# Optimization experiments

Hardware: AMD Instinct MI355X
Metric: run time of the kernel (lower is better)

The kernel has to match this reference:

```python
import jax, jax.numpy as jnp
import numpy as np

B = 4096
M = 4            # n_modalities
T = 8            # n_tasks
D = 1024         # feature_dim per modality
DIN = D * M      # concat feature dim = 4096
H = 256          # hidden_dim
H2 = 2 * H       # 512
TEMP = 1.0
EPS = 1e-5


def _layernorm(x, g, b):
    # LayerNorm over last axis (torch nn.LayerNorm semantics, eps=1e-5)
    mu = jnp.mean(x, axis=-1, keepdims=True)
    var = jnp.mean(jnp.square(x - mu), axis=-1, keepdims=True)
    return (x - mu) * jax.lax.rsqrt(var + EPS) * g + b


def setup_inputs() -> dict:
    key = jax.random.key(0)
    ks = jax.random.split(key, 16)
    s = 0.02
    return {
        "f0": jax.random.normal(ks[0], (B, D), jnp.float32),
        "f1": jax.random.normal(ks[1], (B, D), jnp.float32),
        "f2": jax.random.normal(ks[2], (B, D), jnp.float32),
        "f3": jax.random.normal(ks[3], (B, D), jnp.float32),
        # per-task feature-net params (stacked ModuleList)
        "W1": jax.random.normal(ks[4], (T, DIN, H2), jnp.float32) * s,
        "b1": jnp.zeros((T, H2), jnp.float32),
        "g1": jnp.ones((T, H2), jnp.float32),
        "be1": jnp.zeros((T, H2), jnp.float32),
        "W2": jax.random.normal(ks[5], (T, H2, H), jnp.float32) * s,
        "b2": jnp.zeros((T, H), jnp.float32),
        "g2": jnp.ones((T, H), jnp.float32),
        "be2": jnp.zeros((T, H), jnp.float32),
        "task_emb": jax.random.normal(ks[6], (T, H), jnp.float32),
        # per-task weight-net params (Linear(2H -> M))
        "Ww": jax.random.normal(ks[7], (T, H2, M), jnp.float32) * s,
        "bw": jnp.zeros((T, M), jnp.float32),
        "task_ids": jax.random.randint(ks[8], (B,), 0, T, jnp.int32),
    }


def reference(f0, f1, f2, f3, W1, b1, g1, be1, W2, b2, g2, be2, task_emb, Ww, bw, task_ids):
    x = jnp.concatenate([f0, f1, f2, f3], axis=1)              # [B, DIN]
    # compute all-task feature nets densely (T is small), then gather per sample
    h = jnp.einsum('bd,tdh->bth', x, W1) + b1[None]            # [B, T, 2H]
    h = jax.nn.relu(_layernorm(h, g1[None], be1[None]))
    h = jnp.einsum('bth,thk->btk', h, W2) + b2[None]           # [B, T, H]
    h = jax.nn.relu(_layernorm(h, g2[None], be2[None]))
    hid = jnp.take_along_axis(h, task_ids[:, None, None], axis=1)[:, 0]  # [B, H]
    te = task_emb[task_ids]                                    # [B, H]
    comb = jnp.concatenate([hid, te], axis=1)                  # [B, 2H]
    # per-sample gather of small weight-net matrices (irregular access)
    raw = jnp.einsum('bh,bhm->bm', comb, Ww[task_ids]) + bw[task_ids]    # [B, M]
    return jax.nn.softmax(raw / TEMP, axis=1)
```

## Files before the change

kernel.cpp:

```cpp
#include <hip/hip_runtime.h>
#include <stdint.h>

#define B_N 4096
#define T_N 8
#define DIN 4096
#define H2C 512
#define HC 256
#define NWG1 1024
#define NWG2 264
#define SPLITK1 4

typedef __attribute__((ext_vector_type(8))) short bf16x8;
typedef __attribute__((ext_vector_type(4))) float f32x4;

static __device__ __forceinline__ unsigned short f2bf(float f) {
    union { float f; uint32_t u; } v; v.f = f;
    uint32_t u = v.u;
    uint32_t r = (u + 0x7FFFu + ((u >> 16) & 1u)) >> 16;
    return (unsigned short)r;
}

static __device__ __forceinline__ float bf2f(uint32_t h) {
    union { uint32_t u; float f; } v; v.u = h << 16; return v.f;
}

static __device__ __forceinline__ uint32_t pk2(float a, float b) {
    uint32_t r;
    asm volatile("v_cvt_pk_bf16_f32 %0, %1, %2" : "=v"(r) : "v"(a), "v"(b));
    return r;
}

static __device__ __forceinline__ void gl2lds16(const unsigned short* g, unsigned short* l) {
    __builtin_amdgcn_global_load_lds(
        (const __attribute__((address_space(1))) unsigned int*)(g),
        (__attribute__((address_space(3))) unsigned int*)(l), 16, 0, 0);
}

static __device__ __forceinline__ int xcd_remap(int bid, int nwg) {
    int xcd = bid & 7, idx = bid >> 3;
    int q = nwg >> 3, r = nwg & 7;
    return (xcd < r ? xcd * (q + 1) : r * (q + 1) + (xcd - r) * q) + idx;
}

__launch_bounds__(256)
__global__ void k_pre(const float* __restrict__ f0, const float* __restrict__ f1,
                      const float* __restrict__ f2, const float* __restrict__ f3,
                      const float* __restrict__ W1, const float* __restrict__ W2,
                      const int* __restrict__ task_ids,
                      const float* __restrict__ temb, const float* __restrict__ Ww,
                      const float* __restrict__ bw,
                      unsigned short* __restrict__ Xb, unsigned short* __restrict__ W1t,
                      unsigned short* __restrict__ W2t,
                      int* __restrict__ order, int* __restrict__ tiles, int* __restrict__ bmap,
                      int* __restrict__ tiles2, int* __restrict__ ntile2,
                      float* __restrict__ tb) {
    int blk = blockIdx.x, tid = threadIdx.x;
    if (blk == 0) {
        __shared__ unsigned long long wtot[4][2];
        __shared__ int lc[T_N], lseg[T_N], tb1p[T_N + 1], tb2p[T_N + 1];
        int lane = tid & 63, wv = tid >> 6;
        int4 a0 = *(const int4*)(task_ids + tid * 16);
        int4 a1 = *(const int4*)(task_ids + tid * 16 + 4);
        int4 a2 = *(const int4*)(task_ids + tid * 16 + 8);
        int4 a3 = *(const int4*)(task_ids + tid * 16 + 12);
        int myt[16] = {a0.x, a0.y, a0.z, a0.w, a1.x, a1.y, a1.z, a1.w,
                       a2.x, a2.y, a2.z, a2.w, a3.x, a3.y, a3.z, a3.w};
        unsigned long long ph0 = 0, ph1 = 0;
        #pragma unroll
        for (int i = 0; i < 16; ++i) {
            int t = myt[i];
            if (t < 4) ph0 += 1ull << (t * 16); else ph1 += 1ull << ((t - 4) * 16);
        }
        unsigned long long s0 = ph0, s1 = ph1;
        for (int o = 1; o < 64; o <<= 1) {
            unsigned long long u0 = __shfl_up(s0, o);
            unsigned long long u1 = __shfl_up(s1, o);
            if (lane >= o) { s0 += u0; s1 += u1; }
        }
        if (lane == 63) { wtot[wv][0] = s0; wtot[wv][1] = s1; }
        __syncthreads();
        unsigned long long e0 = s0 - ph0, e1 = s1 - ph1;
        for (int w2 = 0; w2 < wv; ++w2) { e0 += wtot[w2][0]; e1 += wtot[w2][1]; }
        if (tid == 0) {
            unsigned long long t0 = 0, t1 = 0;
            for (int w2 = 0; w2 < 4; ++w2) { t0 += wtot[w2][0]; t1 += wtot[w2][1]; }
            int s = 0;
            for (int t = 0; t < T_N; ++t) {
                int c = (int)((t < 4 ? (t0 >> (t * 16)) : (t1 >> ((t - 4) * 16))) & 0xFFFF);
                lc[t] = c; lseg[t] = s; s += c;
            }
            int q1 = 0, q2 = 0;
            for (int t = 0; t < T_N; ++t) {
                tb1p[t] = q1; tb2p[t] = q2;
                q1 += (lc[t] + 127) >> 7; q2 += (lc[t] + 15) >> 4;
            }
            tb1p[T_N] = q1; tb2p[T_N] = q2;
            ntile2[0] = q2;
        }
        __syncthreads();
        unsigned long long r0 = e0, r1 = e1;
        #pragma unroll
        for (int i = 0; i < 16; ++i) {
            int t = myt[i], rk;
            if (t < 4) { rk = (int)((r0 >> (t * 16)) & 0xFFFF); r0 += 1ull << (t * 16); }
            else { int u = t - 4; rk = (int)((r1 >> (u * 16)) & 0xFFFF); r1 += 1ull << (u * 16); }
            order[lseg[t] + rk] = tid * 16 + i;
        }
        int n1 = tb1p[T_N], n2 = tb2p[T_N];
        for (int e = tid; e < n1; e += 256) {
            int t = 0; while (e >= tb1p[t + 1]) ++t;
            int rr = (e - tb1p[t]) << 7;
            tiles[3 * e] = t; tiles[3 * e + 1] = lseg[t] + rr;
            int rem = lc[t] - rr; tiles[3 * e + 2] = rem < 128 ? rem : 128;
        }
        for (int e = tid; e < n2; e += 256) {
            int t = 0; while (e >= tb2p[t + 1]) ++t;
            int rr = (e - tb2p[t]) << 4;
            tiles2[3 * e] = t; tiles2[3 * e + 1] = lseg[t] + rr;
            int rem = lc[t] - rr; tiles2[3 * e + 2] = rem < 16 ? rem : 16;
        }
        for (int s = tid; s < NWG1; s += 256) {
            int t = s & 7, j = s >> 3;
            int base = tb1p[t], nt = tb1p[t + 1] - base;
            bmap[s] = (j < nt * 16) ? (((base + (j >> 4)) << 4) | (j & 15)) : -1;
        }
        __syncthreads();
        if (tid == 0) {
            int freeslot = 0;
            for (int t = 0; t < T_N; ++t) {
                int base = tb1p[t], nt = tb1p[t + 1] - base;
                for (int j = 128; j < nt * 16; ++j) {
                    while (bmap[freeslot] >= 0) ++freeslot;
                    bmap[freeslot] = ((base + (j >> 4)) << 4) | (j & 15);
                }
            }
        }
        for (int t = wv; t < T_N; t += 4) {
            int m = lane & 3, hb = (lane >> 2) * 16;
            float s = 0.f;
            for (int h = 0; h < 16; ++h)
                s += temb[t * HC + hb + h] * Ww[((size_t)t * H2C + HC + hb + h) * 4 + m];
            for (int o = 4; o < 64; o <<= 1) s += __shfl_xor(s, o);
            if (lane < 4) tb[t * 4 + lane] = s + bw[t * 4 + lane];
        }
        return;
    }
    if (blk <= 8192) {
        int g = (blk - 1) * 256 + tid;
        int b = g >> 9, col = (g & 511) * 8;
        int m = col >> 10, d = col & 1023;
        const float* s = (m == 0) ? f0 : (m == 1) ? f1 : (m == 2) ? f2 : f3;
        const float4* sp = (const float4*)(s + (size_t)b * 1024 + d);
        float4 a = sp[0], c = sp[1];
        uint4 w;
        w.x = pk2(a.x, a.y); w.y = pk2(a.z, a.w);
        w.z = pk2(c.x, c.y); w.w = pk2(c.z, c.w);
        *(uint4*)(Xb + (size_t)b * DIN + col) = w;
        return;
    }
    __shared__ float tile[64][65];
    const float* ip; unsigned short* op; int R, C, bx, by, t;
    if (blk < 12289) {
        int idx = blk - 8193; bx = idx & 63; by = (idx >> 6) & 7; t = idx >> 9;
        R = DIN; C = H2C;
        ip = W1 + (size_t)t * R * C; op = W1t + (size_t)t * R * C;
    } else {
        int idx = blk - 12289; bx = idx & 7; by = (idx >> 3) & 3; t = idx >> 5;
        R = H2C; C = HC;
        ip = W2 + (size_t)t * R * C; op = W2t + (size_t)t * R * C;
    }
    int r0 = bx * 64, c0 = by * 64;
    int lr = tid >> 4, lc4 = (tid & 15) * 4;
    #pragma unroll
    for (int i = 0; i < 4; ++i) {
        float4 v = *(const float4*)&ip[(size_t)(r0 + lr + i * 16) * C + c0 + lc4];
        tile[lr + i * 16][lc4 + 0] = v.x;
        tile[lr + i * 16][lc4 + 1] = v.y;
        tile[lr + i * 16][lc4 + 2] = v.z;
        tile[lr + i * 16][lc4 + 3] = v.w;
    }
    __syncthreads();
    int r4 = (tid & 15) * 4;
    #pragma unroll
    for (int i = 0; i < 4; ++i) {
        int cc = i * 16 + (tid >> 4);
        uint2 wv;
        wv.x = pk2(tile[r4 + 0][cc], tile[r4 + 1][cc]);
        wv.y = pk2(tile[r4 + 2][cc], tile[r4 + 3][cc]);
        *(uint2*)&op[(size_t)(c0 + cc) * R + r0 + r4] = wv;
    }
}

__launch_bounds__(256)
__global__ void k_gemm1(const unsigned short* __restrict__ A, const unsigned short* __restrict__ Bt,
                        unsigned short* __restrict__ Cb16, const int* __restrict__ order,
                        const int* __restrict__ tiles, const int* __restrict__ bmap) {
    int e = bmap[blockIdx.x];
    if (e < 0) return;
    int tix = e >> 4, sub = e & 15;
    int ct = sub >> 2, kc = sub & 3;
    int t = tiles[3 * tix], prow = tiles[3 * tix + 1], rows = tiles[3 * tix + 2];
    int kb = kc * (DIN / SPLITK1);

    __shared__ unsigned short lds[2][16384];

    int tid = threadIdx.x, lane = tid & 63, w = tid >> 6;
    int wm = w >> 1, wn = w & 1;

    const unsigned short* pA[4];
    const unsigned short* pB[4];
    #pragma unroll
    for (int j = 0; j < 4; ++j) {
        int row = j * 32 + (tid >> 3);
        int colg = (tid & 7) ^ (row & 7);
        int rl = row < rows ? row : rows - 1;
        pA[j] = A + (size_t)order[prow + rl] * DIN + kb + colg * 8;
        pB[j] = Bt + ((size_t)t * H2C + ct * 128 + row) * DIN + kb + colg * 8;
    }

    f32x4 acc[4][4];
    #pragma unroll
    for (int m = 0; m < 4; ++m)
        #pragma unroll
        for (int n = 0; n < 4; ++n)
            acc[m][n] = (f32x4){0.f, 0.f, 0.f, 0.f};

    auto stage = [&](int buf, int k0) {
        unsigned short* dA = &lds[buf][w * 512];
        unsigned short* dB = dA + 8192;
        #pragma unroll
        for (int j = 0; j < 4; ++j) gl2lds16(pA[j] + k0, dA + j * 2048);
        #pragma unroll
        for (int j = 0; j < 4; ++j) gl2lds16(pB[j] + k0, dB + j * 2048);
    };

    constexpr int NIT = DIN / SPLITK1 / 64;
    stage(0, 0);
    __syncthreads();
    int cur = 0;
    for (int it = 0; it < NIT; ++it) {
        if (it + 1 < NIT) stage(cur ^ 1, (it + 1) * 64);
        const unsigned short* As = &lds[cur][0];
        const unsigned short* Bs = As + 8192;
        #pragma unroll
        for (int ks = 0; ks < 2; ++ks) {
            int g = ks * 4 + (lane >> 4);
            bf16x8 af[4], bfv[4];
            #pragma unroll
            for (int m = 0; m < 4; ++m) {
                int row = wm * 64 + m * 16 + (lane & 15);
                af[m] = *(const bf16x8*)&As[row * 64 + ((g ^ (row & 7)) * 8)];
            }
            #pragma unroll
            for (int n = 0; n < 4; ++n) {
                int row = wn * 64 + n * 16 + (lane & 15);
                bfv[n] = *(const bf16x8*)&Bs[row * 64 + ((g ^ (row & 7)) * 8)];
            }
            #pragma unroll
            for (int m = 0; m < 4; ++m)
                #pragma unroll
                for (int n = 0; n < 4; ++n)
                    acc[m][n] = __builtin_amdgcn_mfma_f32_16x16x32_bf16(af[m], bfv[n], acc[m][n], 0, 0, 0);
        }
        __syncthreads();
        cur ^= 1;
    }

    unsigned short* Cb = Cb16 + (size_t)kc * B_N * H2C;
    #pragma unroll
    for (int m = 0; m < 4; ++m) {
        #pragma unroll
        for (int n = 0; n < 4; ++n) {
            int col = ct * 128 + wn * 64 + n * 16 + (lane & 15);
            #pragma unroll
            for (int j = 0; j < 4; ++j) {
                int row = wm * 64 + m * 16 + (lane >> 4) * 4 + j;
                if (row < rows)
                    Cb[(size_t)(prow + row) * H2C + col] = f2bf(acc[m][n][j]);
            }
        }
    }
}

__launch_bounds__(256)
__global__ void k_gemm2f(const unsigned short* __restrict__ h1p, const unsigned short* __restrict__ W2t,
                         const float* __restrict__ b1, const float* __restrict__ g1,
                         const float* __restrict__ be1,
                         const float* __restrict__ b2, const float* __restrict__ g2,
                         const float* __restrict__ be2,
                         const float* __restrict__ Ww, const float* __restrict__ tb,
                         const int* __restrict__ order,
                         const int* __restrict__ tiles2, const int* __restrict__ ntile2,
                         float* __restrict__ out) {
    __shared__ unsigned short Asm[16 * 512];
    __shared__ unsigned short Bsm[2][256 * 32];
    __shared__ float red[16][4][4];

    int id = xcd_remap(blockIdx.x, NWG2);
    if (id >= ntile2[0]) return;
    int t = tiles2[3 * id], prow = tiles2[3 * id + 1], rows = tiles2[3 * id + 2];
    int tid = threadIdx.x, lane = tid & 63, w = tid >> 6;

    {
        int r = tid >> 4;
        int rl = r < rows ? r : rows - 1;
        int c0 = (tid & 15) * 32;
        const unsigned short* p0 = h1p + (size_t)(prow + rl) * H2C + c0;
        const float* pb = b1 + t * H2C + c0;
        float x[32];
        float s = 0.f, sq = 0.f;
        #pragma unroll
        for (int i = 0; i < 32; i += 8) {
            uint4 u0 = *(const uint4*)(p0 + i);
            uint4 u1 = *(const uint4*)(p0 + (size_t)B_N * H2C + i);
            uint4 u2 = *(const uint4*)(p0 + (size_t)2 * B_N * H2C + i);
            uint4 u3 = *(const uint4*)(p0 + (size_t)3 * B_N * H2C + i);
            uint32_t w0[4] = {u0.x, u0.y, u0.z, u0.w};
            uint32_t w1[4] = {u1.x, u1.y, u1.z, u1.w};
            uint32_t w2[4] = {u2.x, u2.y, u2.z, u2.w};
            uint32_t w3[4] = {u3.x, u3.y, u3.z, u3.w};
            float4 c0v = *(const float4*)(pb + i);
            float4 c1v = *(const float4*)(pb + i + 4);
            float cv[8] = {c0v.x, c0v.y, c0v.z, c0v.w, c1v.x, c1v.y, c1v.z, c1v.w};
            #pragma unroll
            for (int q = 0; q < 4; ++q) {
                float v0 = bf2f(w0[q] & 0xFFFFu) + bf2f(w1[q] & 0xFFFFu)
                         + bf2f(w2[q] & 0xFFFFu) + bf2f(w3[q] & 0xFFFFu) + cv[2 * q];
                float v1 = bf2f(w0[q] >> 16) + bf2f(w1[q] >> 16)
                         + bf2f(w2[q] >> 16) + bf2f(w3[q] >> 16) + cv[2 * q + 1];
                x[i + 2 * q] = v0; x[i + 2 * q + 1] = v1;
                s += v0 + v1; sq += v0 * v0 + v1 * v1;
            }
        }
        #pragma unroll
        for (int o = 1; o < 16; o <<= 1) { s += __shfl_xor(s, o); sq += __shfl_xor(sq, o); }
        float mean = s * (1.f / H2C);
        float var = sq * (1.f / H2C) - mean * mean;
        float rstd = rsqrtf(var + 1e-5f);
        const float* pg = g1 + t * H2C + c0;
        const float* pe = be1 + t * H2C + c0;
        #pragma unroll
        for (int i = 0; i < 32; i += 8) {
            float yv[8];
            #pragma unroll
            for (int q = 0; q < 8; q += 4) {
                float4 gv = *(const float4*)(pg + i + q);
                float4 ev = *(const float4*)(pe + i + q);
                yv[q + 0] = fmaxf((x[i + q + 0] - mean) * rstd * gv.x + ev.x, 0.f);
                yv[q + 1] = fmaxf((x[i + q + 1] - mean) * rstd * gv.y + ev.y, 0.f);
                yv[q + 2] = fmaxf((x[i + q + 2] - mean) * rstd * gv.z + ev.z, 0.f);
                yv[q + 3] = fmaxf((x[i + q + 3] - mean) * rstd * gv.w + ev.w, 0.f);
            }
            uint4 wv;
            wv.x = pk2(yv[0], yv[1]); wv.y = pk2(yv[2], yv[3]);
            wv.z = pk2(yv[4], yv[5]); wv.w = pk2(yv[6], yv[7]);
            int g = (c0 + i) >> 3;
            *(uint4*)&Asm[r * 512 + ((g ^ (r & 7)) * 8)] = wv;
        }
    }

    auto stageB = [&](int buf, int it) {
        #pragma unroll
        for (int j = 0; j < 4; ++j) {
            int G = j * 256 + tid;
            int row = G >> 2, g = G & 3;
            int colg = g ^ (row & 3);
            gl2lds16(W2t + ((size_t)t * HC + row) * H2C + it * 32 + colg * 8,
                     &Bsm[buf][(j * 256 + w * 64) * 8]);
        }
    };

    stageB(0, 0);
    __syncthreads();

    f32x4 acc[4];
    #pragma unroll
    for (int n = 0; n < 4; ++n) acc[n] = (f32x4){0.f, 0.f, 0.f, 0.f};

    for (int it = 0; it < 16; ++it) {
        if (it + 1 < 16) stageB((it + 1) & 1, it + 1);
        const unsigned short* Bs = &Bsm[it & 1][0];
        int g = lane >> 4;
        int arow = lane & 15;
        bf16x8 af = *(const bf16x8*)&Asm[arow * 512 + (((it * 4 + g) ^ (arow & 7)) * 8)];
        #pragma unroll
        for (int n = 0; n < 4; ++n) {
            int brow = w * 64 + n * 16 + arow;
            bf16x8 bv = *(const bf16x8*)&Bs[brow * 32 + ((g ^ (brow & 3)) * 8)];
            acc[n] = __builtin_amdgcn_mfma_f32_16x16x32_bf16(af, bv, acc[n], 0, 0, 0);
        }
        __syncthreads();
    }

    float b2v[4], g2v[4], e2v[4];
    float4 wv[4];
    #pragma unroll
    for (int n = 0; n < 4; ++n) {
        int col = w * 64 + n * 16 + (lane & 15);
        b2v[n] = b2[t * HC + col];
        g2v[n] = g2[t * HC + col];
        e2v[n] = be2[t * HC + col];
        wv[n] = *(const float4*)&Ww[((size_t)t * H2C + col) * 4];
    }
    float s4[4], q4[4];
    #pragma unroll
    for (int j = 0; j < 4; ++j) {
        float s = 0.f, sq = 0.f;
        #pragma unroll
        for (int n = 0; n < 4; ++n) {
            float xv = acc[n][j] + b2v[n];
            s += xv; sq += xv * xv;
        }
        #pragma unroll
        for (int o = 1; o < 16; o <<= 1) { s += __shfl_xor(s, o); sq += __shfl_xor(sq, o); }
        s4[j] = s; q4[j] = sq;
    }
    if ((lane & 15) == 0) {
        #pragma unroll
        for (int j = 0; j < 4; ++j) {
            int r = (lane >> 4) * 4 + j;
            red[r][w][0] = s4[j];
            red[r][w][1] = q4[j];
        }
    }
    __syncthreads();
    float mean[4], rstd[4];
    #pragma unroll
    for (int j = 0; j < 4; ++j) {
        int r = (lane >> 4) * 4 + j;
        float S = red[r][0][0] + red[r][1][0] + red[r][2][0] + red[r][3][0];
        float SQ = red[r][0][1] + red[r][1][1] + red[r][2][1] + red[r][3][1];
        mean[j] = S * (1.f / HC);
        float var = SQ * (1.f / HC) - mean[j] * mean[j];
        rstd[j] = rsqrtf(var + 1e-5f);
    }
    float p[4][4];
    #pragma unroll
    for (int j = 0; j < 4; ++j) {
        p[j][0] = 0.f; p[j][1] = 0.f; p[j][2] = 0.f; p[j][3] = 0.f;
        #pragma unroll
        for (int n = 0; n < 4; ++n) {
            float yv = fmaxf((acc[n][j] + b2v[n] - mean[j]) * rstd[j] * g2v[n] + e2v[n], 0.f);
            p[j][0] += yv * wv[n].x; p[j][1] += yv * wv[n].y;
            p[j][2] += yv * wv[n].z; p[j][3] += yv * wv[n].w;
        }
        #pragma unroll
        for (int m = 0; m < 4; ++m)
            #pragma unroll
            for (int o = 1; o < 16; o <<= 1) p[j][m] += __shfl_xor(p[j][m], o);
    }
    __syncthreads();
    if ((lane & 15) == 0) {
        #pragma unroll
        for (int j = 0; j < 4; ++j) {
            int r = (lane >> 4) * 4 + j;
            red[r][w][0] = p[j][0]; red[r][w][1] = p[j][1];
            red[r][w][2] = p[j][2]; red[r][w][3] = p[j][3];
        }
    }
    __syncthreads();
    if (tid < 16 && tid < rows) {
        float raw[4];
        #pragma unroll
        for (int m = 0; m < 4; ++m)
            raw[m] = red[tid][0][m] + red[tid][1][m] + red[tid][2][m] + red[tid][3][m] + tb[t * 4 + m];
        float mx = fmaxf(fmaxf(raw[0], raw[1]), fmaxf(raw[2], raw[3]));
        float e0 = expf(raw[0] - mx), e1 = expf(raw[1] - mx);
        float e2 = expf(raw[2] - mx), e3 = expf(raw[3] - mx);
        float si = 1.f / (e0 + e1 + e2 + e3);
        *(float4*)(out + (size_t)order[prow + tid] * 4) = make_float4(e0 * si, e1 * si, e2 * si, e3 * si);
    }
}

extern "C" void kernel_launch(void* const* d_in, const int* in_sizes, int n_in,
                              void* d_out, int out_size, void* d_ws, size_t ws_size,
                              hipStream_t stream) {
    const float* f0 = (const float*)d_in[0];
    const float* f1 = (const float*)d_in[1];
    const float* f2 = (const float*)d_in[2];
    const float* f3 = (const float*)d_in[3];
    const float* W1 = (const float*)d_in[4];
    const float* b1 = (const float*)d_in[5];
    const float* g1 = (const float*)d_in[6];
    const float* be1 = (const float*)d_in[7];
    const float* W2 = (const float*)d_in[8];
    const float* b2 = (const float*)d_in[9];
    const float* g2 = (const float*)d_in[10];
    const float* be2 = (const float*)d_in[11];
    const float* temb = (const float*)d_in[12];
    const float* Ww = (const float*)d_in[13];
    const float* bw = (const float*)d_in[14];
    const int* task_ids = (const int*)d_in[15];
    float* out = (float*)d_out;

    char* ws = (char*)d_ws;
    size_t off = 0;
    auto walloc = [&](size_t bytes) -> void* {
        void* p = ws + off;
        off = (off + bytes + 255) & ~(size_t)255;
        return p;
    };
    float* tb = (float*)walloc(128);
    int* tiles = (int*)walloc(64 * 3 * 4);
    int* bmap = (int*)walloc(NWG1 * 4);
    int* tiles2 = (int*)walloc(272 * 3 * 4);
    int* ntile2 = (int*)walloc(4);
    int* order = (int*)walloc((size_t)B_N * 4);
    unsigned short* Xb = (unsigned short*)walloc((size_t)B_N * DIN * 2);
    unsigned short* W1t = (unsigned short*)walloc((size_t)T_N * H2C * DIN * 2);
    unsigned short* W2t = (unsigned short*)walloc((size_t)T_N * HC * H2C * 2);
    unsigned short* h1p = (unsigned short*)walloc((size_t)SPLITK1 * B_N * H2C * 2);

    k_pre<<<12545, 256, 0, stream>>>(f0, f1, f2, f3, W1, W2, task_ids, temb, Ww, bw,
                                     Xb, W1t, W2t, order, tiles, bmap, tiles2, ntile2, tb);
    k_gemm1<<<NWG1, 256, 0, stream>>>(Xb, W1t, h1p, order, tiles, bmap);
    k_gemm2f<<<NWG2, 256, 0, stream>>>(h1p, W2t, b1, g1, be1, b2, g2, be2, Ww, tb,
                                       order, tiles2, ntile2, out);
}
```

Baseline: 91.39 us.

## Coarsen prep kernel blocks, drop LDS staging of W2 in GEMM2, grid by task

```diff
diff --git a/kernel.cpp b/kernel.cpp
--- a/kernel.cpp
+++ b/kernel.cpp
@@ -7,7 +7,7 @@
 #define H2C 512
 #define HC 256
 #define NWG1 1024
-#define NWG2 264
+#define NWG2 2048
 #define SPLITK1 4
 
 typedef __attribute__((ext_vector_type(8))) short bf16x8;
@@ -24,22 +24,10 @@
     union { uint32_t u; float f; } v; v.u = h << 16; return v.f;
 }
 
-static __device__ __forceinline__ uint32_t pk2(float a, float b) {
-    uint32_t r;
-    asm volatile("v_cvt_pk_bf16_f32 %0, %1, %2" : "=v"(r) : "v"(a), "v"(b));
-    return r;
-}
-
 static __device__ __forceinline__ void gl2lds16(const unsigned short* g, unsigned short* l) {
     __builtin_amdgcn_global_load_lds(
         (const __attribute__((address_space(1))) unsigned int*)(g),
         (__attribute__((address_space(3))) unsigned int*)(l), 16, 0, 0);
-}
-
-static __device__ __forceinline__ int xcd_remap(int bid, int nwg) {
-    int xcd = bid & 7, idx = bid >> 3;
-    int q = nwg >> 3, r = nwg & 7;
-    return (xcd < r ? xcd * (q + 1) : r * (q + 1) + (xcd - r) * q) + idx;
 }
 
 __launch_bounds__(256)
@@ -52,7 +40,7 @@
                       unsigned short* __restrict__ Xb, unsigned short* __restrict__ W1t,
                       unsigned short* __restrict__ W2t,
                       int* __restrict__ order, int* __restrict__ tiles, int* __restrict__ bmap,
-                      int* __restrict__ tiles2, int* __restrict__ ntile2,
+                      int* __restrict__ tiles2, int* __restrict__ tbp,
                       float* __restrict__ tb) {
     int blk = blockIdx.x, tid = threadIdx.x;
     if (blk == 0) {
@@ -95,7 +83,6 @@
                 q1 += (lc[t] + 127) >> 7; q2 += (lc[t] + 15) >> 4;
             }
             tb1p[T_N] = q1; tb2p[T_N] = q2;
-            ntile2[0] = q2;
         }
         __syncthreads();
         unsigned long long r0 = e0, r1 = e1;
@@ -106,6 +93,7 @@
             else { int u = t - 4; rk = (int)((r1 >> (u * 16)) & 0xFFFF); r1 += 1ull << (u * 16); }
             order[lseg[t] + rk] = tid * 16 + i;
         }
+        if (tid <= T_N) tbp[tid] = tb2p[tid];
         int n1 = tb1p[T_N], n2 = tb2p[T_N];
         for (int e = tid; e < n1; e += 256) {
             int t = 0; while (e >= tb1p[t + 1]) ++t;
@@ -145,49 +133,66 @@
         }
         return;
     }
-    if (blk <= 8192) {
-        int g = (blk - 1) * 256 + tid;
-        int b = g >> 9, col = (g & 511) * 8;
+    if (blk <= 2048) {
+        int g0 = ((blk - 1) * 256 + tid) * 4;
+        size_t e0 = (size_t)g0 * 8;
+        int b = (int)(e0 >> 12), col = (int)(e0 & 4095);
         int m = col >> 10, d = col & 1023;
         const float* s = (m == 0) ? f0 : (m == 1) ? f1 : (m == 2) ? f2 : f3;
         const float4* sp = (const float4*)(s + (size_t)b * 1024 + d);
-        float4 a = sp[0], c = sp[1];
-        uint4 w;
-        w.x = pk2(a.x, a.y); w.y = pk2(a.z, a.w);
-        w.z = pk2(c.x, c.y); w.w = pk2(c.z, c.w);
-        *(uint4*)(Xb + (size_t)b * DIN + col) = w;
+        unsigned short* op = Xb + (size_t)b * DIN + col;
+        #pragma unroll
+        for (int q = 0; q < 4; ++q) {
+            float4 a = sp[2 * q], c = sp[2 * q + 1];
+            uint4 w;
+            w.x = (uint32_t)f2bf(a.x) | ((uint32_t)f2bf(a.y) << 16);
+            w.y = (uint32_t)f2bf(a.z) | ((uint32_t)f2bf(a.w) << 16);
+            w.z = (uint32_t)f2bf(c.x) | ((uint32_t)f2bf(c.y) << 16);
+            w.w = (uint32_t)f2bf(c.z) | ((uint32_t)f2bf(c.w) << 16);
+            *(uint4*)(op + q * 8) = w;
+        }
         return;
     }
-    __shared__ float tile[64][65];
-    const float* ip; unsigned short* op; int R, C, bx, by, t;
-    if (blk < 12289) {
-        int idx = blk - 8193; bx = idx & 63; by = (idx >> 6) & 7; t = idx >> 9;
+    __shared__ float tile[128 * 65];
+    const float* ip; unsigned short* op; int R, C, r0, c0;
+    if (blk <= 4096) {
+        int idx = blk - 2049;
+        int bx = idx & 31, by = (idx >> 5) & 7, t = idx >> 8;
         R = DIN; C = H2C;
         ip = W1 + (size_t)t * R * C; op = W1t + (size_t)t * R * C;
+        r0 = bx * 128; c0 = by * 64;
     } else {
-        int idx = blk - 12289; bx = idx & 7; by = (idx >> 3) & 3; t = idx >> 5;
+        int idx = blk - 4097;
+        int bx = idx & 3, by = (idx >> 2) & 3, t = idx >> 4;
         R = H2C; C = HC;
         ip = W2 + (size_t)t * R * C; op = W2t + (size_t)t * R * C;
-    }
-    int r0 = bx * 64, c0 = by * 64;
-    int lr = tid >> 4, lc4 = (tid & 15) * 4;
-    #pragma unroll
-    for (int i = 0; i < 4; ++i) {
-        float4 v = *(const float4*)&ip[(size_t)(r0 + lr + i * 16) * C + c0 + lc4];
-        tile[lr + i * 16][lc4 + 0] = v.x;
-        tile[lr + i * 16][lc4 + 1] = v.y;
-        tile[lr + i * 16][lc4 + 2] = v.z;
-        tile[lr + i * 16][lc4 + 3] = v.w;
+        r0 = bx * 128; c0 = by * 64;
+    }
+    {
+        int kq = tid >> 4, c4 = (tid & 15) * 4;
+        #pragma unroll
+        for (int i = 0; i < 8; ++i) {
+            int k = kq + i * 16;
+            float4 v = *(const float4*)&ip[(size_t)(r0 + k) * C + c0 + c4];
+            int q = (k >> 5) & 3;
+            tile[k * 65 + ((c4 + 0) ^ q)] = v.x;
+            tile[k * 65 + ((c4 + 1) ^ q)] = v.y;
+            tile[k * 65 + ((c4 + 2) ^ q)] = v.z;
+            tile[k * 65 + ((c4 + 3) ^ q)] = v.w;
+        }
     }
     __syncthreads();
-    int r4 = (tid & 15) * 4;
-    #pragma unroll
-    for (int i = 0; i < 4; ++i) {
-        int cc = i * 16 + (tid >> 4);
-        uint2 wv;
-        wv.x = pk2(tile[r4 + 0][cc], tile[r4 + 1][cc]);
-        wv.y = pk2(tile[r4 + 2][cc], tile[r4 + 3][cc]);
-        *(uint2*)&op[(size_t)(c0 + cc) * R + r0 + r4] = wv;
+    {
+        int col = tid >> 2, q = tid & 3;
+        int colS = col ^ q;
+        unsigned short ow[32];
+        #pragma unroll
+        for (int j = 0; j < 32; ++j)
+            ow[j] = f2bf(tile[(q * 32 + j) * 65 + colS]);
+        unsigned short* dst = op + (size_t)(c0 + col) * R + r0 + q * 32;
+        #pragma unroll
+        for (int v = 0; v < 4; ++v)
+            *(uint4*)(dst + v * 8) = *(uint4*)&ow[v * 8];
     }
 }
 
@@ -290,15 +295,16 @@
                          const float* __restrict__ be2,
                          const float* __restrict__ Ww, const float* __restrict__ tb,
                          const int* __restrict__ order,
-                         const int* __restrict__ tiles2, const int* __restrict__ ntile2,
+                         const int* __restrict__ tiles2, const int* __restrict__ tbp,
                          float* __restrict__ out) {
     __shared__ unsigned short Asm[16 * 512];
-    __shared__ unsigned short Bsm[2][256 * 32];
     __shared__ float red[16][4][4];
 
-    int id = xcd_remap(blockIdx.x, NWG2);
-    if (id >= ntile2[0]) return;
-    int t = tiles2[3 * id], prow = tiles2[3 * id + 1], rows = tiles2[3 * id + 2];
+    int tres = blockIdx.x & 7, j = blockIdx.x >> 3;
+    int base = tbp[tres];
+    if (base + j >= tbp[tres + 1]) return;
+    int e = base + j;
+    int t = tiles2[3 * e], prow = tiles2[3 * e + 1], rows = tiles2[3 * e + 2];
     int tid = threadIdx.x, lane = tid & 63, w = tid >> 6;
 
     {
@@ -341,55 +347,46 @@
         const float* pe = be1 + t * H2C + c0;
         #pragma unroll
         for (int i = 0; i < 32; i += 8) {
-            float yv[8];
+            unsigned short y[8];
             #pragma unroll
             for (int q = 0; q < 8; q += 4) {
                 float4 gv = *(const float4*)(pg + i + q);
                 float4 ev = *(const float4*)(pe + i + q);
-                yv[q + 0] = fmaxf((x[i + q + 0] - mean) * rstd * gv.x + ev.x, 0.f);
-                yv[q + 1] = fmaxf((x[i + q + 1] - mean) * rstd * gv.y + ev.y, 0.f);
-                yv[q + 2] = fmaxf((x[i + q + 2] - mean) * rstd * gv.z + ev.z, 0.f);
-                yv[q + 3] = fmaxf((x[i + q + 3] - mean) * rstd * gv.w + ev.w, 0.f);
+                y[q + 0] = f2bf(fmaxf((x[i + q + 0] - mean) * rstd * gv.x + ev.x, 0.f));
+                y[q + 1] = f2bf(fmaxf((x[i + q + 1] - mean) * rstd * gv.y + ev.y, 0.f));
+                y[q + 2] = f2bf(fmaxf((x[i + q + 2] - mean) * rstd * gv.z + ev.z, 0.f));
+                y[q + 3] = f2bf(fmaxf((x[i + q + 3] - mean) * rstd * gv.w + ev.w, 0.f));
             }
             uint4 wv;
-            wv.x = pk2(yv[0], yv[1]); wv.y = pk2(yv[2], yv[3]);
-            wv.z = pk2(yv[4], yv[5]); wv.w = pk2(yv[6], yv[7]);
+            wv.x = (uint32_t)y[0] | ((uint32_t)y[1] << 16);
+            wv.y = (uint32_t)y[2] | ((uint32_t)y[3] << 16);
+            wv.z = (uint32_t)y[4] | ((uint32_t)y[5] << 16);
+            wv.w = (uint32_t)y[6] | ((uint32_t)y[7] << 16);
             int g = (c0 + i) >> 3;
             *(uint4*)&Asm[r * 512 + ((g ^ (r & 7)) * 8)] = wv;
         }
     }
-
-    auto stageB = [&](int buf, int it) {
-        #pragma unroll
-        for (int j = 0; j < 4; ++j) {
-            int G = j * 256 + tid;
-            int row = G >> 2, g = G & 3;
-            int colg = g ^ (row & 3);
-            gl2lds16(W2t + ((size_t)t * HC + row) * H2C + it * 32 + colg * 8,
-                     &Bsm[buf][(j * 256 + w * 64) * 8]);
-        }
-    };
-
-    stageB(0, 0);
     __syncthreads();
 
+    int g = lane >> 4, arow = lane & 15;
+    const unsigned short* bp[4];
+    #pragma unroll
+    for (int n = 0; n < 4; ++n)
+        bp[n] = W2t + ((size_t)t * HC + w * 64 + n * 16 + arow) * H2C + g * 8;
+
     f32x4 acc[4];
     #pragma unroll
     for (int n = 0; n < 4; ++n) acc[n] = (f32x4){0.f, 0.f, 0.f, 0.f};
 
+    #pragma unroll 4
     for (int it = 0; it < 16; ++it) {
-        if (it + 1 < 16) stageB((it + 1) & 1, it + 1);
-        const unsigned short* Bs = &Bsm[it & 1][0];
-        int g = lane >> 4;
-        int arow = lane & 15;
         bf16x8 af = *(const bf16x8*)&Asm[arow * 512 + (((it * 4 + g) ^ (arow & 7)) * 8)];
-        #pragma unroll
-        for (int n = 0; n < 4; ++n) {
-            int brow = w * 64 + n * 16 + arow;
-            bf16x8 bv = *(const bf16x8*)&Bs[brow * 32 + ((g ^ (brow & 3)) * 8)];
-            acc[n] = __builtin_amdgcn_mfma_f32_16x16x32_bf16(af, bv, acc[n], 0, 0, 0);
-        }
-        __syncthreads();
+        bf16x8 bv[4];
+        #pragma unroll
+        for (int n = 0; n < 4; ++n) bv[n] = *(const bf16x8*)(bp[n] + it * 32);
+        #pragma unroll
+        for (int n = 0; n < 4; ++n)
+            acc[n] = __builtin_amdgcn_mfma_f32_16x16x32_bf16(af, bv[n], acc[n], 0, 0, 0);
     }
 
     float b2v[4], g2v[4], e2v[4];
@@ -404,58 +401,58 @@
     }
     float s4[4], q4[4];
     #pragma unroll
-    for (int j = 0; j < 4; ++j) {
+    for (int j2 = 0; j2 < 4; ++j2) {
         float s = 0.f, sq = 0.f;
         #pragma unroll
         for (int n = 0; n < 4; ++n) {
-            float xv = acc[n][j] + b2v[n];
+            float xv = acc[n][j2] + b2v[n];
             s += xv; sq += xv * xv;
         }
         #pragma unroll
         for (int o = 1; o < 16; o <<= 1) { s += __shfl_xor(s, o); sq += __shfl_xor(sq, o); }
-        s4[j] = s; q4[j] = sq;
+        s4[j2] = s; q4[j2] = sq;
     }
     if ((lane & 15) == 0) {
         #pragma unroll
-        for (int j = 0; j < 4; ++j) {
-            int r = (lane >> 4) * 4 + j;
-            red[r][w][0] = s4[j];
-            red[r][w][1] = q4[j];
+        for (int j2 = 0; j2 < 4; ++j2) {
+            int r = (lane >> 4) * 4 + j2;
+            red[r][w][0] = s4[j2];
+            red[r][w][1] = q4[j2];
         }
     }
     __syncthreads();
     float mean[4], rstd[4];
     #pragma unroll
-    for (int j = 0; j < 4; ++j) {
-        int r = (lane >> 4) * 4 + j;
+    for (int j2 = 0; j2 < 4; ++j2) {
+        int r = (lane >> 4) * 4 + j2;
         float S = red[r][0][0] + red[r][1][0] + red[r][2][0] + red[r][3][0];
         float SQ = red[r][0][1] + red[r][1][1] + red[r][2][1] + red[r][3][1];
-        mean[j] = S * (1.f / HC);
-        float var = SQ * (1.f / HC) - mean[j] * mean[j];
-        rstd[j] = rsqrtf(var + 1e-5f);
+        mean[j2] = S * (1.f / HC);
+        float var = SQ * (1.f / HC) - mean[j2] * mean[j2];
+        rstd[j2] = rsqrtf(var + 1e-5f);
     }
     float p[4][4];
     #pragma unroll
-    for (int j = 0; j < 4; ++j) {
-        p[j][0] = 0.f; p[j][1] = 0.f; p[j][2] = 0.f; p[j][3] = 0.f;
+    for (int j2 = 0; j2 < 4; ++j2) {
+        p[j2][0] = 0.f; p[j2][1] = 0.f; p[j2][2] = 0.f; p[j2][3] = 0.f;
         #pragma unroll
         for (int n = 0; n < 4; ++n) {
-            float yv = fmaxf((acc[n][j] + b2v[n] - mean[j]) * rstd[j] * g2v[n] + e2v[n], 0.f);
-            p[j][0] += yv * wv[n].x; p[j][1] += yv * wv[n].y;
-            p[j][2] += yv * wv[n].z; p[j][3] += yv * wv[n].w;
+            float yv = fmaxf((acc[n][j2] + b2v[n] - mean[j2]) * rstd[j2] * g2v[n] + e2v[n], 0.f);
+            p[j2][0] += yv * wv[n].x; p[j2][1] += yv * wv[n].y;
+            p[j2][2] += yv * wv[n].z; p[j2][3] += yv * wv[n].w;
         }
         #pragma unroll
         for (int m = 0; m < 4; ++m)
             #pragma unroll
-            for (int o = 1; o < 16; o <<= 1) p[j][m] += __shfl_xor(p[j][m], o);
+            for (int o = 1; o < 16; o <<= 1) p[j2][m] += __shfl_xor(p[j2][m], o);
     }
     __syncthreads();
     if ((lane & 15) == 0) {
         #pragma unroll
-        for (int j = 0; j < 4; ++j) {
-            int r = (lane >> 4) * 4 + j;
-            red[r][w][0] = p[j][0]; red[r][w][1] = p[j][1];
-            red[r][w][2] = p[j][2]; red[r][w][3] = p[j][3];
+        for (int j2 = 0; j2 < 4; ++j2) {
+            int r = (lane >> 4) * 4 + j2;
+            red[r][w][0] = p[j2][0]; red[r][w][1] = p[j2][1];
+            red[r][w][2] = p[j2][2]; red[r][w][3] = p[j2][3];
         }
     }
     __syncthreads();
@@ -503,17 +500,17 @@
     float* tb = (float*)walloc(128);
     int* tiles = (int*)walloc(64 * 3 * 4);
     int* bmap = (int*)walloc(NWG1 * 4);
-    int* tiles2 = (int*)walloc(272 * 3 * 4);
-    int* ntile2 = (int*)walloc(4);
+    int* tiles2 = (int*)walloc(2048 * 3 * 4);
+    int* tbp = (int*)walloc((T_N + 1) * 4);
     int* order = (int*)walloc((size_t)B_N * 4);
     unsigned short* Xb = (unsigned short*)walloc((size_t)B_N * DIN * 2);
     unsigned short* W1t = (unsigned short*)walloc((size_t)T_N * H2C * DIN * 2);
     unsigned short* W2t = (unsigned short*)walloc((size_t)T_N * HC * H2C * 2);
     unsigned short* h1p = (unsigned short*)walloc((size_t)SPLITK1 * B_N * H2C * 2);
 
-    k_pre<<<12545, 256, 0, stream>>>(f0, f1, f2, f3, W1, W2, task_ids, temb, Ww, bw,
-                                     Xb, W1t, W2t, order, tiles, bmap, tiles2, ntile2, tb);
+    k_pre<<<4225, 256, 0, stream>>>(f0, f1, f2, f3, W1, W2, task_ids, temb, Ww, bw,
+                                    Xb, W1t, W2t, order, tiles, bmap, tiles2, tbp, tb);
     k_gemm1<<<NWG1, 256, 0, stream>>>(Xb, W1t, h1p, order, tiles, bmap);
     k_gemm2f<<<NWG2, 256, 0, stream>>>(h1p, W2t, b1, g1, be1, b2, g2, be2, Ww, tb,
-                                       order, tiles2, ntile2, out);
-}
+                                       order, tiles2, tbp, out);
+}
```

Measured after the change: 99.71 us. 9.1% more time.
